# Optimization experiments

Measured on AMD Instinct MI355X. Metric: run time of the kernel, lower is better.

## Reference

```python
import jax, jax.numpy as jnp
import numpy as np

N_WAY = 5
K_SHOT = 5
NBNN_TOPK = 3
TEMPERATURE = 2.0
EPS = 1e-8


def setup_inputs() -> dict:
    key = jax.random.key(0)
    k1, k2, k3 = jax.random.split(key, 3)
    b, q, c, h, w = 4, 75, 640, 11, 11
    s = N_WAY * K_SHOT
    support_xf = jax.random.normal(k1, (b, s, c, h, w), jnp.float32)
    query_xf = jax.random.normal(k2, (b, q, c, h, w), jnp.float32)
    # episodes are ordered class-major: [way0 shots..., way1 shots..., ...]
    support_y = jnp.tile(jnp.repeat(jnp.arange(N_WAY, dtype=jnp.int32), K_SHOT)[None, :], (b, 1))
    query_y = jax.random.randint(k3, (b, q), 0, N_WAY, dtype=jnp.int32)
    return {"support_xf": support_xf, "query_xf": query_xf,
            "support_y": support_y, "query_y": query_y}


def _mn4_loss(support_xf, query_xf, query_y):
    b, s, c, h, w = support_xf.shape
    q = query_xf.shape[1]
    M_q = h * w
    M_s = K_SHOT * h * w

    # ---- InnerproductSimilarity (cosine) ----
    # support: [b, N, c, M_s]  (class-major grouping of shots)
    sf = support_xf.reshape(b, N_WAY, K_SHOT, c, h * w).transpose(0, 1, 3, 2, 4).reshape(b, N_WAY, c, M_s)
    qf = query_xf.reshape(b, q, c, M_q)
    sf = sf / (jnp.linalg.norm(sf, axis=2, keepdims=True) + EPS)
    qf = qf / (jnp.linalg.norm(qf, axis=2, keepdims=True) + EPS)
    # simi: [b, q, N, M_q, M_s]
    simi = jnp.einsum('bqcm,bncs->bqnms', qf, sf)

    # ---- _MNN (compensate_for_single=True branch) ----
    # merged view: [b, q, M_q, N*M_s]
    merged = simi.transpose(0, 1, 3, 2, 4).reshape(b, q, M_q, N_WAY * M_s)
    query_nearest = jnp.argmax(merged, axis=-1)          # [b, q, M_q]
    class_wise_max = simi.max(-1).max(2) + 1.0           # [b, q, M_q]
    class_m = jax.nn.one_hot(query_nearest, N_WAY * M_s, dtype=simi.dtype) * class_wise_max[..., None]
    support_nearest = jnp.argmax(class_m, axis=-2)       # [b, q, N*M_s]
    gathered = jnp.take_along_axis(support_nearest, query_nearest, axis=-1)  # [b, q, M_q]
    q_mask = (gathered == jnp.arange(M_q)[None, None, :])                    # [b, q, M_q]

    # ---- NBNN value: topk over support descriptors, masked sum over query descriptors ----
    topv = jax.lax.top_k(simi, NBNN_TOPK)[0].mean(-1)    # [b, q, N, M_q]
    query_value = (topv * q_mask[:, :, None, :].astype(topv.dtype)).sum(-1)  # [b, q, N]
    logits = query_value.reshape(b * q, N_WAY) / TEMPERATURE

    # ---- cross entropy (mean) ----
    logp = jax.nn.log_softmax(logits, axis=-1)
    y = query_y.reshape(-1)
    loss = -jnp.take_along_axis(logp, y[:, None], axis=1).mean()
    return loss


def reference(support_xf, query_xf, support_y, query_y):
    del support_y  # episodes are class-major by construction
    return _mn4_loss(support_xf, query_xf, query_y)
```

## Files before the change

### kernel.cpp

```cpp
#include <hip/hip_runtime.h>
#include <hip/hip_bf16.h>
#include <math.h>

#define BB 4
#define QQ 75
#define NBQ 300
#define CC 640
#define HW 121
#define NW 5
#define KS 5
#define SS 25
#define MS 605
#define JT 3025
#define BQ_PER_XCD 38

typedef __attribute__((ext_vector_type(8))) short short8;
typedef __attribute__((ext_vector_type(4))) float f32x4;

#define OFF_SBF   0
#define SBF_F     (BB*JT*CC/2)
#define OFF_QBF   (OFF_SBF + SBF_F)
#define QBF_F     (NBQ*HW*CC/2)
#define OFF_P     (OFF_QBF + QBF_F)

__device__ __forceinline__ void async16(const void* g, void* l) {
    __builtin_amdgcn_global_load_lds(
        (const __attribute__((address_space(1))) unsigned int*)g,
        (__attribute__((address_space(3))) unsigned int*)l, 16, 0, 0);
}

__global__ void prep_kernel(const float* __restrict__ sup, const float* __restrict__ qry,
                            __hip_bfloat16* __restrict__ Sbf, __hip_bfloat16* __restrict__ Qbf,
                            float* __restrict__ out)
{
    const int col = blockIdx.x;
    const int t   = threadIdx.x;
    if (col == 0 && t == 0) out[0] = 0.f;
    const float* src;
    __hip_bfloat16* dst;
    if (col < BB * SS) {
        const int b = col / SS, s = col % SS;
        const int n = s / KS, k = s % KS;
        src = sup + (size_t)col * (CC * HW);
        dst = Sbf + ((size_t)b * JT + n * MS + k * HW) * CC;
    } else {
        const int bq = col - BB * SS;
        src = qry + (size_t)bq * (CC * HW);
        dst = Qbf + (size_t)bq * (HW * CC);
    }

    __shared__ float inv[128];
    __shared__ float T[32][128];

    const int cc2 = t >> 7, hw1 = t & 127;
    float ss0 = 0.f, ss1 = 0.f;
    if (hw1 < HW) {
        const float* p = src + hw1;
#pragma unroll 16
        for (int c = cc2; c < CC; c += 4) {
            float v0 = p[(size_t)c * HW];
            float v1 = p[(size_t)(c + 2) * HW];
            ss0 = fmaf(v0, v0, ss0);
            ss1 = fmaf(v1, v1, ss1);
        }
    }
    T[cc2][hw1] = ss0 + ss1;
    __syncthreads();
    if (t < 128) inv[t] = (t < HW) ? 1.f / (sqrtf(T[0][t] + T[1][t]) + 1e-8f) : 0.f;

    for (int c0 = 0; c0 < CC; c0 += 32) {
        __syncthreads();
#pragma unroll
        for (int i = 0; i < 16; ++i) {
            int idx = t + i * 256;
            int cc = idx >> 7, hw = idx & 127;
            if (hw < HW) T[cc][hw] = src[(size_t)(c0 + cc) * HW + hw] * inv[hw];
        }
        __syncthreads();
        const int hw = t >> 1, half = t & 1;
        if (hw < HW) {
            __hip_bfloat16 hv[16];
#pragma unroll
            for (int i = 0; i < 16; ++i) hv[i] = __float2bfloat16(T[half * 16 + i][hw]);
            int4* op = reinterpret_cast<int4*>(dst + (size_t)hw * CC + c0 + half * 16);
            op[0] = reinterpret_cast<int4*>(hv)[0];
            op[1] = reinterpret_cast<int4*>(hv)[1];
        }
    }
}

__launch_bounds__(256, 2)
__global__ void simi_kernel(const __hip_bfloat16* __restrict__ Sbf,
                            const __hip_bfloat16* __restrict__ Qbf,
                            float4* __restrict__ pout)
{
    const int xcd   = blockIdx.x & 7;
    const int local = blockIdx.x >> 3;
    const int n     = local % NW;
    const int bq    = xcd * BQ_PER_XCD + local / NW;
    if (bq >= NBQ) return;
    const int b   = bq / QQ;
    const int tid = threadIdx.x;
    const int lane = tid & 63, wid = tid >> 6;
    const int l15 = lane & 15, l4 = lane >> 4;
    const int wr0 = (wid & 1) * 64;
    const int wc0 = (wid >> 1) * 64;

    const unsigned short* qbase = (const unsigned short*)(Qbf + (size_t)bq * (HW * CC));
    const unsigned short* sbase = (const unsigned short*)(Sbf + ((size_t)b * JT + n * MS) * CC);

    __shared__ __align__(16) unsigned short AsBuf[2][128 * 64];
    __shared__ __align__(16) unsigned short BsBuf[2][128 * 64];

    const int srow = lane >> 3;
    const int kb   = (lane & 7) ^ srow;
    int aoff[4];
#pragma unroll
    for (int p = 0; p < 4; ++p) {
        int arow = wid * 32 + p * 8 + srow;
        int grow = arow < HW ? arow : HW - 1;
        aoff[p] = grow * CC + kb * 8;
    }
    const int ldso_base = wid * 4096 + lane * 16;

#define STAGE(ms0_, c0_, nb_)                                                        \
    {                                                                                \
        _Pragma("unroll")                                                            \
        for (int p = 0; p < 4; ++p) {                                                \
            const int ldso = ldso_base + p * 1024;                                   \
            async16(qbase + aoff[p] + (c0_), (char*)&AsBuf[nb_][0] + ldso);          \
            int j_ = (ms0_) + wid * 32 + p * 8 + srow;                               \
            int jc_ = j_ < MS ? j_ : MS - 1;                                         \
            async16(sbase + jc_ * CC + kb * 8 + (c0_), (char*)&BsBuf[nb_][0] + ldso);\
        }                                                                            \
    }

    float rt0[16], rt1[16], rt2[16]; int ra[16];
#pragma unroll
    for (int i = 0; i < 16; ++i) { rt0[i] = -INFINITY; rt1[i] = -INFINITY; rt2[i] = -INFINITY; ra[i] = 0; }

    STAGE(0, 0, 0);
    __syncthreads();
    int nb = 0;

    for (int ms0 = 0; ms0 < MS; ms0 += 128) {
        f32x4 acc[4][4];
#pragma unroll
        for (int mi = 0; mi < 4; ++mi)
#pragma unroll
            for (int ni = 0; ni < 4; ++ni)
#pragma unroll
                for (int r = 0; r < 4; ++r) acc[mi][ni][r] = 0.f;

        for (int c0 = 0; c0 < CC; c0 += 64) {
            int nc = c0 + 64, nms = ms0;
            if (nc == CC) { nc = 0; nms = ms0 + 128; }
            if (nms < MS) STAGE(nms, nc, nb ^ 1);

#pragma unroll
            for (int ks = 0; ks < 2; ++ks) {
                const int slot = (ks * 4 + l4) ^ (l15 & 7);
                short8 af[4], bf[4];
#pragma unroll
                for (int mi = 0; mi < 4; ++mi)
                    af[mi] = *(const short8*)(&AsBuf[nb][0] + (wr0 + mi * 16 + l15) * 64 + slot * 8);
#pragma unroll
                for (int ni = 0; ni < 4; ++ni)
                    bf[ni] = *(const short8*)(&BsBuf[nb][0] + (wc0 + ni * 16 + l15) * 64 + slot * 8);
#pragma unroll
                for (int mi = 0; mi < 4; ++mi)
#pragma unroll
                    for (int ni = 0; ni < 4; ++ni)
                        acc[mi][ni] = __builtin_amdgcn_mfma_f32_16x16x32_bf16(
                            af[mi], bf[ni], acc[mi][ni], 0, 0, 0);
            }
            nb ^= 1;
            __syncthreads();
        }

        int jg[4]; bool jvalid[4];
#pragma unroll
        for (int nf = 0; nf < 4; ++nf) {
            const int jl = ms0 + wc0 + nf * 16 + l15;
            jvalid[nf] = (jl < MS);
            jg[nf] = n * MS + jl;
        }
#pragma unroll
        for (int mi = 0; mi < 4; ++mi)
#pragma unroll
            for (int nf = 0; nf < 4; ++nf)
#pragma unroll
                for (int r = 0; r < 4; ++r) {
                    const int si = mi * 4 + r;
                    float v = jvalid[nf] ? acc[mi][nf][r] : -INFINITY;
                    const bool gt = v > rt0[si];
                    ra[si] = gt ? jg[nf] : ra[si];
                    const float m1 = fminf(rt0[si], v);
                    rt0[si] = fmaxf(rt0[si], v);
                    const float m2 = fminf(rt1[si], m1);
                    rt1[si] = fmaxf(rt1[si], m1);
                    rt2[si] = fmaxf(rt2[si], m2);
                }
    }

#pragma unroll
    for (int si = 0; si < 16; ++si) {
#pragma unroll
        for (int mask = 1; mask <= 8; mask <<= 1) {
            const float o0 = __shfl_xor(rt0[si], mask);
            const float o1 = __shfl_xor(rt1[si], mask);
            const float o2 = __shfl_xor(rt2[si], mask);
            const int   oa = __shfl_xor(ra[si],  mask);
            const bool take = (o0 > rt0[si]) || (o0 == rt0[si] && oa < ra[si]);
            ra[si] = take ? oa : ra[si];
            float m1 = fminf(rt0[si], o0); rt0[si] = fmaxf(rt0[si], o0);
            float m2 = fminf(rt1[si], m1); rt1[si] = fmaxf(rt1[si], m1);
            rt2[si] = fmaxf(rt2[si], m2);
            m1 = fminf(rt0[si], o1); rt0[si] = fmaxf(rt0[si], o1);
            m2 = fminf(rt1[si], m1); rt1[si] = fmaxf(rt1[si], m1);
            rt2[si] = fmaxf(rt2[si], m2);
            m1 = fminf(rt0[si], o2); rt0[si] = fmaxf(rt0[si], o2);
            m2 = fminf(rt1[si], m1); rt1[si] = fmaxf(rt1[si], m1);
            rt2[si] = fmaxf(rt2[si], m2);
        }
    }

    float s0 = rt0[0], s1 = rt1[0], s2 = rt2[0]; int sa = ra[0];
#pragma unroll
    for (int i = 1; i < 16; ++i) {
        const bool p = (l15 == i);
        s0 = p ? rt0[i] : s0; s1 = p ? rt1[i] : s1; s2 = p ? rt2[i] : s2; sa = p ? ra[i] : sa;
    }
    const int m = wr0 + (l15 >> 2) * 16 + l4 * 4 + (l15 & 3);

    __syncthreads();
    float4* mbuf = (float4*)&AsBuf[0][0];
    if ((wid >> 1) == 0) {
        float4 v; v.x = s0; v.y = s1; v.z = s2; v.w = __int_as_float(sa);
        mbuf[m] = v;
    }
    __syncthreads();
    if ((wid >> 1) == 1) {
        const float4 o = mbuf[m];
        const int oa = __float_as_int(o.w);
        const bool take = (o.x > s0) || (o.x == s0 && oa < sa);
        sa = take ? oa : sa;
        float m1 = fminf(s0, o.x); s0 = fmaxf(s0, o.x);
        float m2 = fminf(s1, m1);  s1 = fmaxf(s1, m1);
        s2 = fmaxf(s2, m2);
        m1 = fminf(s0, o.y); s0 = fmaxf(s0, o.y);
        m2 = fminf(s1, m1);  s1 = fmaxf(s1, m1);
        s2 = fmaxf(s2, m2);
        m1 = fminf(s0, o.z); s0 = fmaxf(s0, o.z);
        m2 = fminf(s1, m1);  s1 = fmaxf(s1, m1);
        s2 = fmaxf(s2, m2);
        if (m < HW) {
            float4 v; v.x = s0; v.y = s1; v.z = s2; v.w = __int_as_float(sa);
            pout[(bq * NW + n) * HW + m] = v;
        }
    }
#undef STAGE
}

__global__ void merge_kernel(const float4* __restrict__ pout, const int* __restrict__ qy,
                             float* __restrict__ out)
{
    const int bq  = blockIdx.x;
    const int tid = threadIdx.x;

    __shared__ float cw[128];
    __shared__ int   ag[128];
    __shared__ float tv[NW][128];
    __shared__ float maskf[128];
    __shared__ float lg[8];

    if (tid < HW) {
        float g0 = -INFINITY; int garg = 0;
#pragma unroll
        for (int n = 0; n < NW; ++n) {
            const float4 a = pout[(bq * NW + n) * HW + tid];
            if (a.x > g0) { g0 = a.x; garg = __float_as_int(a.w); }
            tv[n][tid] = (a.x + a.y + a.z) * (1.f / 3.f);
        }
        cw[tid] = g0 + 1.0f;
        ag[tid] = garg;
    }
    __syncthreads();
    if (tid < HW) {
        const float mycw = cw[tid];
        const int   myag = ag[tid];
        float ok = 1.f;
        for (int m2 = 0; m2 < HW; ++m2) {
            if (m2 == tid) continue;
            if (ag[m2] == myag) {
                float c2 = cw[m2];
                if (c2 > mycw || (c2 == mycw && m2 < tid)) ok = 0.f;
            }
        }
        maskf[tid] = ok;
    }
    __syncthreads();
    if (tid < NW) {
        float s = 0.f;
        for (int mq = 0; mq < HW; ++mq) s += maskf[mq] * tv[tid][mq];
        lg[tid] = s * 0.5f;
    }
    __syncthreads();
    if (tid == 0) {
        float m = lg[0];
#pragma unroll
        for (int n2 = 1; n2 < NW; ++n2) m = fmaxf(m, lg[n2]);
        float se = 0.f;
#pragma unroll
        for (int n2 = 0; n2 < NW; ++n2) se += expf(lg[n2] - m);
        int y = qy[bq];
        atomicAdd(out, -(lg[y] - m - logf(se)) * (1.f / NBQ));
    }
}

extern "C" void kernel_launch(void* const* d_in, const int* in_sizes, int n_in,
                              void* d_out, int out_size, void* d_ws, size_t ws_size,
                              hipStream_t stream)
{
    const float* sup = (const float*)d_in[0];
    const float* qry = (const float*)d_in[1];
    const int*   qy  = (const int*)d_in[3];
    float* out = (float*)d_out;
    float* ws  = (float*)d_ws;

    __hip_bfloat16* Sbf = (__hip_bfloat16*)(ws + OFF_SBF);
    __hip_bfloat16* Qbf = (__hip_bfloat16*)(ws + OFF_QBF);
    float4* pout = (float4*)(ws + OFF_P);

    hipLaunchKernelGGL(prep_kernel, dim3(BB * SS + NBQ), dim3(256), 0, stream,
                       sup, qry, Sbf, Qbf, out);
    hipLaunchKernelGGL(simi_kernel, dim3(8 * BQ_PER_XCD * NW), dim3(256), 0, stream,
                       Sbf, Qbf, pout);
    hipLaunchKernelGGL(merge_kernel, dim3(NBQ), dim3(128), 0, stream, pout, qy, out);
}
```

Before: 454.2 us.

## Load query A-fragments directly from global, drop A LDS buffer, raise occupancy

The query operand tile is no longer staged through shared memory. Each wave now loads its MFMA A-fragments directly from global memory, relying on L1/L2 caching since the same query rows are reused across the support column blocks. This halves the LDS footprint, and launch bounds are raised to allow three blocks per SM. In exchange, global loads sit synchronously on the critical path inside the K loop, with no async prefetch, and the extra register pressure could cause spills.

Measured after the change: 948.2 us. +108.8%, slower.

```diff
diff --git a/kernel.cpp b/kernel.cpp
--- a/kernel.cpp
+++ b/kernel.cpp
@@ -89,7 +89,7 @@
     }
 }
 
-__launch_bounds__(256, 2)
+__launch_bounds__(256, 3)
 __global__ void simi_kernel(const __hip_bfloat16* __restrict__ Sbf,
                             const __hip_bfloat16* __restrict__ Qbf,
                             float4* __restrict__ pout)
@@ -109,29 +109,28 @@
     const unsigned short* qbase = (const unsigned short*)(Qbf + (size_t)bq * (HW * CC));
     const unsigned short* sbase = (const unsigned short*)(Sbf + ((size_t)b * JT + n * MS) * CC);
 
-    __shared__ __align__(16) unsigned short AsBuf[2][128 * 64];
     __shared__ __align__(16) unsigned short BsBuf[2][128 * 64];
 
     const int srow = lane >> 3;
     const int kb   = (lane & 7) ^ srow;
+    const int ldso_base = wid * 4096 + lane * 16;
+
     int aoff[4];
 #pragma unroll
-    for (int p = 0; p < 4; ++p) {
-        int arow = wid * 32 + p * 8 + srow;
-        int grow = arow < HW ? arow : HW - 1;
-        aoff[p] = grow * CC + kb * 8;
-    }
-    const int ldso_base = wid * 4096 + lane * 16;
-
-#define STAGE(ms0_, c0_, nb_)                                                        \
+    for (int mi = 0; mi < 4; ++mi) {
+        int row = wr0 + mi * 16 + l15;
+        if (row > HW - 1) row = HW - 1;
+        aoff[mi] = row * CC + l4 * 8;
+    }
+
+#define STAGE_B(ms0_, c0_, nb_)                                                      \
     {                                                                                \
         _Pragma("unroll")                                                            \
         for (int p = 0; p < 4; ++p) {                                                \
-            const int ldso = ldso_base + p * 1024;                                   \
-            async16(qbase + aoff[p] + (c0_), (char*)&AsBuf[nb_][0] + ldso);          \
             int j_ = (ms0_) + wid * 32 + p * 8 + srow;                               \
             int jc_ = j_ < MS ? j_ : MS - 1;                                         \
-            async16(sbase + jc_ * CC + kb * 8 + (c0_), (char*)&BsBuf[nb_][0] + ldso);\
+            async16(sbase + jc_ * CC + kb * 8 + (c0_),                               \
+                    (char*)&BsBuf[nb_][0] + ldso_base + p * 1024);                   \
         }                                                                            \
     }
 
@@ -139,7 +138,7 @@
 #pragma unroll
     for (int i = 0; i < 16; ++i) { rt0[i] = -INFINITY; rt1[i] = -INFINITY; rt2[i] = -INFINITY; ra[i] = 0; }
 
-    STAGE(0, 0, 0);
+    STAGE_B(0, 0, 0);
     __syncthreads();
     int nb = 0;
 
@@ -155,15 +154,19 @@
         for (int c0 = 0; c0 < CC; c0 += 64) {
             int nc = c0 + 64, nms = ms0;
             if (nc == CC) { nc = 0; nms = ms0 + 128; }
-            if (nms < MS) STAGE(nms, nc, nb ^ 1);
+            if (nms < MS) STAGE_B(nms, nc, nb ^ 1);
+
+            short8 af[2][4];
+#pragma unroll
+            for (int ks = 0; ks < 2; ++ks)
+#pragma unroll
+                for (int mi = 0; mi < 4; ++mi)
+                    af[ks][mi] = *(const short8*)(qbase + aoff[mi] + c0 + ks * 32);
 
 #pragma unroll
             for (int ks = 0; ks < 2; ++ks) {
                 const int slot = (ks * 4 + l4) ^ (l15 & 7);
-                short8 af[4], bf[4];
-#pragma unroll
-                for (int mi = 0; mi < 4; ++mi)
-                    af[mi] = *(const short8*)(&AsBuf[nb][0] + (wr0 + mi * 16 + l15) * 64 + slot * 8);
+                short8 bf[4];
 #pragma unroll
                 for (int ni = 0; ni < 4; ++ni)
                     bf[ni] = *(const short8*)(&BsBuf[nb][0] + (wc0 + ni * 16 + l15) * 64 + slot * 8);
@@ -172,7 +175,7 @@
 #pragma unroll
                     for (int ni = 0; ni < 4; ++ni)
                         acc[mi][ni] = __builtin_amdgcn_mfma_f32_16x16x32_bf16(
-                            af[mi], bf[ni], acc[mi][ni], 0, 0, 0);
+                            af[ks][mi], bf[ni], acc[mi][ni], 0, 0, 0);
             }
             nb ^= 1;
             __syncthreads();
@@ -234,7 +237,7 @@
     const int m = wr0 + (l15 >> 2) * 16 + l4 * 4 + (l15 & 3);
 
     __syncthreads();
-    float4* mbuf = (float4*)&AsBuf[0][0];
+    float4* mbuf = (float4*)&BsBuf[0][0];
     if ((wid >> 1) == 0) {
         float4 v; v.x = s0; v.y = s1; v.z = s2; v.w = __int_as_float(sa);
         mbuf[m] = v;
@@ -259,7 +262,7 @@
             pout[(bq * NW + n) * HW + m] = v;
         }
     }
-#undef STAGE
+#undef STAGE_B
 }
 
 __global__ void merge_kernel(const float4* __restrict__ pout, const int* __restrict__ qy,
```
